# Performance work log

Measured on AMD Instinct MI355X. Metric: run time of the kernel, lower is better.

Reference implementation:

```python
import jax, jax.numpy as jnp
import numpy as np

NUM_HEADS = 8
MAXN = 1.0 - 1e-5        # ball projection radius for |k|=1
ATANH_CLIP = 1.0 - 1e-7  # artanh argument clamp (geoopt-style)
MIN_DEN = 1e-15

def _sqnorm(x):
    return jnp.sum(x * x, axis=-1, keepdims=True)

def _norm(x):
    return jnp.sqrt(jnp.clip(_sqnorm(x), MIN_DEN))

def artanh(x):
    return jnp.arctanh(jnp.clip(x, -ATANH_CLIP, ATANH_CLIP))

def project(x):
    n = _norm(x)
    return jnp.where(n > MAXN, x * (MAXN / n), x)

def mobius_add(x, y):
    # Mobius addition on Poincare ball, k=-1
    x2, y2 = _sqnorm(x), _sqnorm(y)
    xy = jnp.sum(x * y, axis=-1, keepdims=True)
    num = (1.0 + 2.0 * xy + y2) * x + (1.0 - x2) * y
    den = 1.0 + 2.0 * xy + x2 * y2
    return num / jnp.maximum(den, MIN_DEN)

def mobius_matvec(W, x):
    xn = jnp.clip(_norm(x), MIN_DEN)
    mx = x @ W.T
    mxn = jnp.clip(_norm(mx), MIN_DEN)
    res = jnp.tanh(mxn / xn * artanh(xn)) * (mx / mxn)
    zero = jnp.all(mx == 0, axis=-1, keepdims=True)
    return jnp.where(zero, jnp.zeros_like(res), res)

def mobius_linear(x, W, b):
    return project(mobius_add(mobius_matvec(W, x), b))

def logmap0(y):
    yn = jnp.clip(_norm(y), MIN_DEN)
    return artanh(yn) * y / yn

def expmap0(u):
    un = jnp.clip(_norm(u), MIN_DEN)
    return jnp.tanh(un) * u / un

def _fwd(query, key, value, Wq, bq, Wk, bk, Wv, bv, Wo, bo):
    B, S, D = query.shape
    dk = D // NUM_HEADS
    heads = lambda x: x.reshape(B, S, NUM_HEADS, dk).transpose(0, 2, 1, 3)
    Q = heads(mobius_linear(query, Wq, bq))  # (B,H,S,dk)
    K = heads(mobius_linear(key, Wk, bk))
    V = heads(mobius_linear(value, Wv, bv))
    # pairwise Poincare distance dist(q,k) = 2*artanh(||(-q) (+) k||),
    # expanded via dot products so we never build a (B,H,S,S,dk) tensor
    x2 = _sqnorm(Q)                          # (B,H,S,1)
    y2 = jnp.swapaxes(_sqnorm(K), -1, -2)    # (B,H,1,S)
    xy = jnp.einsum('bhid,bhjd->bhij', Q, K)
    A = 1.0 - 2.0 * xy + y2                  # coeff of (-q)
    Bc = 1.0 - x2                            # coeff of k
    num2 = A * A * x2 + Bc * Bc * y2 - 2.0 * A * Bc * xy
    den = jnp.maximum(1.0 - 2.0 * xy + x2 * y2, MIN_DEN)
    dist = 2.0 * artanh(jnp.sqrt(jnp.clip(num2, 0.0)) / den)
    scores = -dist / np.sqrt(dk).astype(np.float32)
    attn = jax.nn.softmax(scores, axis=-1)   # dropout skipped (eval/deterministic)
    # gyromidpoint weighted sum (vectorized form of the original python loops):
    # all softmax weights are > 0, so every j passes the >1e-10 branch
    w = attn / (jnp.sum(attn, axis=-1, keepdims=True) + 1e-10)
    mid = jnp.einsum('bhij,bhjd->bhid', w, logmap0(V))
    out = expmap0(mid)
    out = out.transpose(0, 2, 1, 3).reshape(B, S, D)
    return mobius_linear(out, Wo, bo), attn


def setup_inputs() -> dict:
    key = jax.random.key(0)
    ks = jax.random.split(key, 12)
    B, S, D = 2, 2048, 512
    pt = lambda k: project(0.05 * jax.random.normal(k, (B, S, D), dtype=jnp.float32))
    inp = {'query': pt(ks[0]), 'key': pt(ks[1]), 'value': pt(ks[2])}
    wscale = 1.0 / np.sqrt(D)
    for i, nm in enumerate(['q', 'k', 'v', 'o']):
        inp['W' + nm] = wscale * jax.random.normal(ks[3 + i], (D, D), dtype=jnp.float32)
        inp['b' + nm] = project(0.01 * jax.random.normal(ks[7 + i], (D,), dtype=jnp.float32))
    return inp


def reference(query, key, value, Wq, bq, Wk, bk, Wv, bv, Wo, bo):
    return _fwd(query, key, value, Wq, bq, Wk, bk, Wv, bv, Wo, bo)
```

## Files before the change

kernel.cpp:

```cpp
#include <hip/hip_runtime.h>
#include <math.h>

namespace {

constexpr int kB  = 2;
constexpr int kS  = 2048;
constexpr int kD  = 512;
constexpr int kH  = 8;
constexpr int kDK = 64;
constexpr int kM  = kB * kS;
constexpr int kBH = kB * kH;

typedef __attribute__((ext_vector_type(8))) short bf16x8;
typedef __attribute__((ext_vector_type(4))) float f32x4;

__device__ __forceinline__ float wave_sum64(float v) {
#pragma unroll
    for (int o = 32; o > 0; o >>= 1) v += __shfl_xor(v, o, 64);
    return v;
}

__device__ __forceinline__ unsigned short f2bf(float f) {
    unsigned u = __float_as_uint(f);
    unsigned r = (u + 0x7FFF + ((u >> 16) & 1)) >> 16;
    return (unsigned short)r;
}
__device__ __forceinline__ float bf2f(unsigned short h) {
    return __uint_as_float(((unsigned)h) << 16);
}

#define MAXN_F  ((float)(1.0 - 1e-5))
#define ACLIP_F ((float)(1.0 - 1e-7))

__global__ __launch_bounds__(256) void gemm_mfma(const float* __restrict__ X,
                                                 const float* __restrict__ W,
                                                 float* __restrict__ Y) {
    __shared__ unsigned short Ah[64 * 64], Al[64 * 64], Bh[64 * 64], Bl[64 * 64];
    const int m0 = blockIdx.x * 64;
    const int n0 = blockIdx.y * 64;
    const int tid = threadIdx.x;
    const int w = tid >> 6, l = tid & 63;
    const int lr = l & 15, lh = l >> 4;
    const int sr = tid >> 2;
    const int sk = (tid & 3) * 16;
    float4 xr[4], wr[4];
#pragma unroll
    for (int i = 0; i < 4; ++i) {
        xr[i] = *(const float4*)(X + (size_t)(m0 + sr) * 512 + sk + i * 4);
        wr[i] = *(const float4*)(W + (size_t)(n0 + sr) * 512 + sk + i * 4);
    }
    f32x4 acc[4];
#pragma unroll
    for (int j = 0; j < 4; ++j) acc[j] = (f32x4){0.f, 0.f, 0.f, 0.f};

    for (int c = 0; c < 8; ++c) {
        if (c) __syncthreads();
        {
            unsigned hx[8], lx[8], hw_[8], lw_[8];
#pragma unroll
            for (int t = 0; t < 8; ++t) {
                float e0 = ((const float*)&xr[t >> 1])[(t & 1) * 2 + 0];
                float e1 = ((const float*)&xr[t >> 1])[(t & 1) * 2 + 1];
                unsigned short h0 = f2bf(e0), h1 = f2bf(e1);
                hx[t] = (unsigned)h0 | ((unsigned)h1 << 16);
                lx[t] = (unsigned)f2bf(e0 - bf2f(h0)) | ((unsigned)f2bf(e1 - bf2f(h1)) << 16);
                float f0 = ((const float*)&wr[t >> 1])[(t & 1) * 2 + 0];
                float f1 = ((const float*)&wr[t >> 1])[(t & 1) * 2 + 1];
                unsigned short g0 = f2bf(f0), g1 = f2bf(f1);
                hw_[t] = (unsigned)g0 | ((unsigned)g1 << 16);
                lw_[t] = (unsigned)f2bf(f0 - bf2f(g0)) | ((unsigned)f2bf(f1 - bf2f(g1)) << 16);
            }
            const int ga = (sk >> 3) ^ (sr & 7);
            const int gb = ((sk >> 3) + 1) ^ (sr & 7);
            *(uint4*)&Ah[sr * 64 + ga * 8] = make_uint4(hx[0], hx[1], hx[2], hx[3]);
            *(uint4*)&Ah[sr * 64 + gb * 8] = make_uint4(hx[4], hx[5], hx[6], hx[7]);
            *(uint4*)&Al[sr * 64 + ga * 8] = make_uint4(lx[0], lx[1], lx[2], lx[3]);
            *(uint4*)&Al[sr * 64 + gb * 8] = make_uint4(lx[4], lx[5], lx[6], lx[7]);
            *(uint4*)&Bh[sr * 64 + ga * 8] = make_uint4(hw_[0], hw_[1], hw_[2], hw_[3]);
            *(uint4*)&Bh[sr * 64 + gb * 8] = make_uint4(hw_[4], hw_[5], hw_[6], hw_[7]);
            *(uint4*)&Bl[sr * 64 + ga * 8] = make_uint4(lw_[0], lw_[1], lw_[2], lw_[3]);
            *(uint4*)&Bl[sr * 64 + gb * 8] = make_uint4(lw_[4], lw_[5], lw_[6], lw_[7]);
        }
        if (c < 7) {
            const int k1 = (c + 1) * 64;
#pragma unroll
            for (int i = 0; i < 4; ++i) {
                xr[i] = *(const float4*)(X + (size_t)(m0 + sr) * 512 + k1 + sk + i * 4);
                wr[i] = *(const float4*)(W + (size_t)(n0 + sr) * 512 + k1 + sk + i * 4);
            }
        }
        __syncthreads();
#pragma unroll
        for (int ks = 0; ks < 2; ++ks) {
            const int kb = ks * 4 + lh;
            const int row = w * 16 + lr;
            const int aoff = row * 64 + ((kb ^ (row & 7)) << 3);
            bf16x8 ah = *(const bf16x8*)&Ah[aoff];
            bf16x8 al = *(const bf16x8*)&Al[aoff];
#pragma unroll
            for (int fn = 0; fn < 4; ++fn) {
                const int col = fn * 16 + lr;
                const int boff = col * 64 + ((kb ^ (col & 7)) << 3);
                bf16x8 bh8 = *(const bf16x8*)&Bh[boff];
                bf16x8 bl8 = *(const bf16x8*)&Bl[boff];
                acc[fn] = __builtin_amdgcn_mfma_f32_16x16x32_bf16(ah, bh8, acc[fn], 0, 0, 0);
                acc[fn] = __builtin_amdgcn_mfma_f32_16x16x32_bf16(al, bh8, acc[fn], 0, 0, 0);
                acc[fn] = __builtin_amdgcn_mfma_f32_16x16x32_bf16(ah, bl8, acc[fn], 0, 0, 0);
            }
        }
    }
#pragma unroll
    for (int fn = 0; fn < 4; ++fn)
#pragma unroll
        for (int r = 0; r < 4; ++r)
            Y[(size_t)(m0 + w * 16 + lh * 4 + r) * 512 + n0 + fn * 16 + lr] = acc[fn][r];
}

__global__ __launch_bounds__(256) void rowops(const float* __restrict__ X,
                                              const float* __restrict__ MX,
                                              const float* __restrict__ bvec,
                                              float* __restrict__ out) {
    __shared__ float4 red4[4];
    __shared__ float red1[4];
    const int row = blockIdx.x;
    const int tid = threadIdx.x;
    const float2 xv = ((const float2*)(X + (size_t)row * kD))[tid];
    const float2 mv = ((const float2*)(MX + (size_t)row * kD))[tid];
    const float2 bv = ((const float2*)bvec)[tid];
    float sx  = fmaf(xv.x, xv.x, xv.y * xv.y);
    float sm  = fmaf(mv.x, mv.x, mv.y * mv.y);
    float smb = fmaf(mv.x, bv.x, mv.y * bv.y);
    float sb  = fmaf(bv.x, bv.x, bv.y * bv.y);
#pragma unroll
    for (int o = 32; o > 0; o >>= 1) {
        sx  += __shfl_xor(sx, o, 64);
        sm  += __shfl_xor(sm, o, 64);
        smb += __shfl_xor(smb, o, 64);
        sb  += __shfl_xor(sb, o, 64);
    }
    if ((tid & 63) == 0) red4[tid >> 6] = make_float4(sx, sm, smb, sb);
    __syncthreads();
    {
        float4 r0 = red4[0], r1 = red4[1], r2 = red4[2], r3 = red4[3];
        sx  = r0.x + r1.x + r2.x + r3.x;
        sm  = r0.y + r1.y + r2.y + r3.y;
        smb = r0.z + r1.z + r2.z + r3.z;
        sb  = r0.w + r1.w + r2.w + r3.w;
    }
    float xn  = sqrtf(fmaxf(sx, 1e-15f));
    float mxn = sqrtf(fmaxf(sm, 1e-15f));
    float xc  = fminf(xn, ACLIP_F);
    float at  = 0.5f * logf((1.f + xc) / (1.f - xc));
    float sc  = tanhf(mxn / xn * at) / mxn;
    if (sm == 0.f) sc = 0.f;
    float x2 = sc * sc * sm;
    float xy = sc * smb;
    float y2 = sb;
    float c1 = 1.f + 2.f * xy + y2;
    float c2 = 1.f - x2;
    float den = fmaxf(1.f + 2.f * xy + x2 * y2, 1e-15f);
    float idn = 1.f / den;
    float ux = (c1 * sc * mv.x + c2 * bv.x) * idn;
    float uy = (c1 * sc * mv.y + c2 * bv.y) * idn;
    float su = wave_sum64(fmaf(ux, ux, uy * uy));
    if ((tid & 63) == 0) red1[tid >> 6] = su;
    __syncthreads();
    su = (red1[0] + red1[1]) + (red1[2] + red1[3]);
    float n = sqrtf(fmaxf(su, 1e-15f));
    float f = (n > MAXN_F) ? (MAXN_F / n) : 1.f;
    ((float2*)(out + (size_t)row * kD))[tid] = make_float2(ux * f, uy * f);
}

__global__ __launch_bounds__(256) void prep2(const float* __restrict__ Qp,
                                             const float* __restrict__ Kp,
                                             const float* __restrict__ Vp,
                                             float* __restrict__ qn2,
                                             float* __restrict__ kn2,
                                             unsigned short* __restrict__ LVbT) {
    __shared__ unsigned short T[64][66];
    const int bh = blockIdx.x >> 5;
    const int k0 = (blockIdx.x & 31) * 64;
    const int b = bh >> 3, h = bh & 7;
    const int w = threadIdx.x >> 6, l = threadIdx.x & 63;
#pragma unroll 4
    for (int i = 0; i < 16; ++i) {
        const int s = k0 + w * 16 + i;
        const size_t src = (size_t)(b * kS + s) * kD + h * kDK + l;
        float qv = Qp[src], kv = Kp[src], vv = Vp[src];
        float sq = wave_sum64(qv * qv);
        float sk = wave_sum64(kv * kv);
        float sv = wave_sum64(vv * vv);
        if (l == 0) { qn2[(bh << 11) + s] = sq; kn2[(bh << 11) + s] = sk; }
        float yn = sqrtf(fmaxf(sv, 1e-15f));
        float yc = fminf(yn, ACLIP_F);
        float coef = 0.5f * logf((1.f + yc) / (1.f - yc)) / yn;
        T[l][w * 16 + i] = f2bf(vv * coef);
    }
    __syncthreads();
    const int n = threadIdx.x >> 2, kk = (threadIdx.x & 3) * 16;
    const unsigned int* Tr = (const unsigned int*)&T[n][kk];
    unsigned int u0 = Tr[0], u1 = Tr[1], u2 = Tr[2], u3 = Tr[3];
    unsigned int u4 = Tr[4], u5 = Tr[5], u6 = Tr[6], u7 = Tr[7];
    unsigned short* dst = LVbT + (((size_t)(bh * 64 + n)) << 11) + k0 + kk;
    *(uint4*)dst = make_uint4(u0, u1, u2, u3);
    *(uint4*)(dst + 8) = make_uint4(u4, u5, u6, u7);
}

__global__ __launch_bounds__(256) void split_qk(const float* __restrict__ Qp,
                                                const float* __restrict__ Kp,
                                                unsigned short* __restrict__ Qhi,
                                                unsigned short* __restrict__ Qlo,
                                                unsigned short* __restrict__ Khi,
                                                unsigned short* __restrict__ Klo) {
    const int gid  = blockIdx.x * 4 + (threadIdx.x >> 6);
    const int lane = threadIdx.x & 63;
    const int bh = gid >> 11, s = gid & 2047;
    const int b = bh >> 3, h = bh & 7;
    const size_t src = (size_t)(b * kS + s) * kD + h * kDK + lane;
    const size_t dst = ((size_t)gid << 6) + lane;
    float qv = Qp[src];
    unsigned short qh = f2bf(qv);
    Qhi[dst] = qh;
    Qlo[dst] = f2bf(qv - bf2f(qh));
    float kv = Kp[src];
    unsigned short kh = f2bf(kv);
    Khi[dst] = kh;
    Klo[dst] = f2bf(kv - bf2f(kh));
}

__global__ __launch_bounds__(256) void fused_attn(const unsigned short* __restrict__ Qhi,
                                                  const unsigned short* __restrict__ Qlo,
                                                  const unsigned short* __restrict__ Khi,
                                                  const unsigned short* __restrict__ Klo,
                                                  const unsigned short* __restrict__ LVbT,
                                                  const float* __restrict__ qn2,
                                                  const float* __restrict__ kn2,
                                                  float* __restrict__ attn,
                                                  float* __restrict__ outcat) {
    __shared__ unsigned short KshH[64 * 64], KshL[64 * 64], LVsh[64 * 64], Psh[32 * 64];
    __shared__ float epl[32 * 68];
    __shared__ float kn2s[2048];
    __shared__ float qn2s[32];
    __shared__ float rsL[4][32], nsL[4][32];
    __shared__ float invSL[32], coefL[32];

    const int wgid = blockIdx.x;
    const int x = wgid & 7, bq_ = wgid >> 3;
    const int bh = 2 * x + (bq_ >> 6);
    const int i0 = (bq_ & 63) * 32;
    const int b = bh >> 3, h = bh & 7;
    const int tid = threadIdx.x;
    const int w = tid >> 6, l = tid & 63;
    const int lr = l & 15, lh = l >> 4;
    const int srj = tid >> 2;
    const int skk = (tid & 3) * 16;
    const size_t kvbase = ((size_t)(bh << 11)) << 6;
    const size_t lvbase = ((size_t)bh) << 17;

    {
        const float* src = kn2 + (bh << 11) + tid * 8;
        *(float4*)&kn2s[tid * 8]     = *(const float4*)src;
        *(float4*)&kn2s[tid * 8 + 4] = *(const float4*)(src + 4);
        if (tid < 32) qn2s[tid] = qn2[(bh << 11) + i0 + tid];
    }
    bf16x8 qah[2][2], qal[2][2];
#pragma unroll
    for (int fm = 0; fm < 2; ++fm)
#pragma unroll
        for (int ks = 0; ks < 2; ++ks) {
            const size_t a = ((size_t)(bh << 11) + i0 + fm * 16 + lr) * 64 + (ks * 4 + lh) * 8;
            qah[fm][ks] = *(const bf16x8*)&Qhi[a];
            qal[fm][ks] = *(const bf16x8*)&Qlo[a];
        }

    const int ga = (((skk >> 3) ^ (srj & 7)) << 3);
    const int gb = ((((skk >> 3) + 1) ^ (srj & 7)) << 3);
    const int jc = w * 16 + lr;
    uint4 pA0, pA1, pB0, pB1, pC0, pC1;
    {
        const unsigned short* kh = Khi + kvbase + (size_t)srj * 64 + skk;
        const unsigned short* kl = Klo + kvbase + (size_t)srj * 64 + skk;
        const unsigned short* lv = LVbT + lvbase + (size_t)srj * 2048 + skk;
        pA0 = *(const uint4*)kh; pA1 = *(const uint4*)(kh + 8);
        pB0 = *(const uint4*)kl; pB1 = *(const uint4*)(kl + 8);
        pC0 = *(const uint4*)lv; pC1 = *(const uint4*)(lv + 8);
    }

    f32x4 pvacc[2];
    pvacc[0] = (f32x4){0.f, 0.f, 0.f, 0.f};
    pvacc[1] = (f32x4){0.f, 0.f, 0.f, 0.f};
    float rsp[2][4] = {};

    for (int t = 0; t < 32; ++t) {
        const int j0 = t * 64;
        if (t) __syncthreads();
        *(uint4*)&KshH[srj * 64 + ga] = pA0; *(uint4*)&KshH[srj * 64 + gb] = pA1;
        *(uint4*)&KshL[srj * 64 + ga] = pB0; *(uint4*)&KshL[srj * 64 + gb] = pB1;
        *(uint4*)&LVsh[srj * 64 + ga] = pC0; *(uint4*)&LVsh[srj * 64 + gb] = pC1;
        if (t < 31) {
            const unsigned short* kh = Khi + kvbase + (size_t)(j0 + 64 + srj) * 64 + skk;
            const unsigned short* kl = Klo + kvbase + (size_t)(j0 + 64 + srj) * 64 + skk;
            const unsigned short* lv = LVbT + lvbase + (size_t)srj * 2048 + j0 + 64 + skk;
            pA0 = *(const uint4*)kh; pA1 = *(const uint4*)(kh + 8);
            pB0 = *(const uint4*)kl; pB1 = *(const uint4*)(kl + 8);
            pC0 = *(const uint4*)lv; pC1 = *(const uint4*)(lv + 8);
        }
        __syncthreads();
        f32x4 sacc[2];
        sacc[0] = (f32x4){0.f, 0.f, 0.f, 0.f};
        sacc[1] = (f32x4){0.f, 0.f, 0.f, 0.f};
#pragma unroll
        for (int ks = 0; ks < 2; ++ks) {
            const int kb = ks * 4 + lh;
            const int boff = jc * 64 + ((kb ^ (jc & 7)) << 3);
            bf16x8 bh8 = *(const bf16x8*)&KshH[boff];
            bf16x8 bl8 = *(const bf16x8*)&KshL[boff];
#pragma unroll
            for (int fm = 0; fm < 2; ++fm) {
                sacc[fm] = __builtin_amdgcn_mfma_f32_16x16x32_bf16(qah[fm][ks], bh8, sacc[fm], 0, 0, 0);
                sacc[fm] = __builtin_amdgcn_mfma_f32_16x16x32_bf16(qal[fm][ks], bh8, sacc[fm], 0, 0, 0);
                sacc[fm] = __builtin_amdgcn_mfma_f32_16x16x32_bf16(qah[fm][ks], bl8, sacc[fm], 0, 0, 0);
            }
        }
        const float y2 = kn2s[j0 + jc];
        const int pg = jc >> 3, pw = jc & 7;
#pragma unroll
        for (int fm = 0; fm < 2; ++fm)
#pragma unroll
            for (int r = 0; r < 4; ++r) {
                const int row = fm * 16 + lh * 4 + r;
                float xy = sacc[fm][r];
                float x2 = qn2s[row];
                float A_ = 1.f - 2.f * xy + y2;
                float Bc = 1.f - x2;
                float num2 = A_ * A_ * x2 + Bc * Bc * y2 - 2.f * A_ * Bc * xy;
                float den  = fmaxf(1.f - 2.f * xy + x2 * y2, 1e-15f);
                float sn   = __builtin_amdgcn_sqrtf(fmaxf(num2, 0.f));
                float dm   = den - sn;
                dm = fmaxf(dm, (den + sn) * 5e-8f);
                float rr = (den + sn) * __builtin_amdgcn_rcpf(dm);
                float e = __builtin_amdgcn_exp2f(-0.125f * __builtin_amdgcn_logf(rr));
                rsp[fm][r] += e;
                Psh[row * 64 + ((pg ^ (row & 7)) << 3) + pw] = f2bf(e);
            }
        __syncthreads();
#pragma unroll
        for (int ks = 0; ks < 2; ++ks) {
            const int kb = ks * 4 + lh;
            bf16x8 bv8 = *(const bf16x8*)&LVsh[jc * 64 + ((kb ^ (jc & 7)) << 3)];
#pragma unroll
            for (int fm = 0; fm < 2; ++fm) {
                const int prow = fm * 16 + lr;
                bf16x8 pa = *(const bf16x8*)&Psh[prow * 64 + ((kb ^ (prow & 7)) << 3)];
                pvacc[fm] = __builtin_amdgcn_mfma_f32_16x16x32_bf16(pa, bv8, pvacc[fm], 0, 0, 0);
            }
        }
    }
    __syncthreads();
#pragma unroll
    for (int fm = 0; fm < 2; ++fm)
#pragma unroll
        for (int r = 0; r < 4; ++r) {
            float v = rsp[fm][r];
            v += __shfl_xor(v, 1, 64); v += __shfl_xor(v, 2, 64);
            v += __shfl_xor(v, 4, 64); v += __shfl_xor(v, 8, 64);
            rsp[fm][r] = v;
        }
    if (lr == 0) {
#pragma unroll
        for (int fm = 0; fm < 2; ++fm)
#pragma unroll
            for (int r = 0; r < 4; ++r) rsL[w][fm * 16 + lh * 4 + r] = rsp[fm][r];
    }
    __syncthreads();
    if (tid < 32) invSL[tid] = 1.f / (rsL[0][tid] + rsL[1][tid] + rsL[2][tid] + rsL[3][tid]);
    __syncthreads();
    float mval[2][4];
#pragma unroll
    for (int fm = 0; fm < 2; ++fm)
#pragma unroll
        for (int r = 0; r < 4; ++r) {
            const int row = fm * 16 + lh * 4 + r;
            float m = pvacc[fm][r] * invSL[row];
            mval[fm][r] = m;
            float ns = m * m;
            ns += __shfl_xor(ns, 1, 64); ns += __shfl_xor(ns, 2, 64);
            ns += __shfl_xor(ns, 4, 64); ns += __shfl_xor(ns, 8, 64);
            if (lr == 0) nsL[w][row] = ns;
        }
    __syncthreads();
    if (tid < 32) {
        float ns = nsL[0][tid] + nsL[1][tid] + nsL[2][tid] + nsL[3][tid];
        float un = sqrtf(fmaxf(ns, 1e-15f));
        coefL[tid] = tanhf(un) / un;
    }
    __syncthreads();
#pragma unroll
    for (int fm = 0; fm < 2; ++fm)
#pragma unroll
        for (int r = 0; r < 4; ++r) {
            const int row = fm * 16 + lh * 4 + r;
            outcat[(size_t)(b * kS + i0 + row) * kD + h * kDK + jc] = mval[fm][r] * coefL[row];
        }

    {
        const unsigned short* kh = Khi + kvbase + (size_t)srj * 64 + skk;
        const unsigned short* kl = Klo + kvbase + (size_t)srj * 64 + skk;
        pA0 = *(const uint4*)kh; pA1 = *(const uint4*)(kh + 8);
        pB0 = *(const uint4*)kl; pB1 = *(const uint4*)(kl + 8);
    }
    for (int t = 0; t < 32; ++t) {
        const int j0 = t * 64;
        __syncthreads();
        *(uint4*)&KshH[srj * 64 + ga] = pA0; *(uint4*)&KshH[srj * 64 + gb] = pA1;
        *(uint4*)&KshL[srj * 64 + ga] = pB0; *(uint4*)&KshL[srj * 64 + gb] = pB1;
        if (t < 31) {
            const unsigned short* kh = Khi + kvbase + (size_t)(j0 + 64 + srj) * 64 + skk;
            const unsigned short* kl = Klo + kvbase + (size_t)(j0 + 64 + srj) * 64 + skk;
            pA0 = *(const uint4*)kh; pA1 = *(const uint4*)(kh + 8);
            pB0 = *(const uint4*)kl; pB1 = *(const uint4*)(kl + 8);
        }
        __syncthreads();
        f32x4 sacc[2];
        sacc[0] = (f32x4){0.f, 0.f, 0.f, 0.f};
        sacc[1] = (f32x4){0.f, 0.f, 0.f, 0.f};
#pragma unroll
        for (int ks = 0; ks < 2; ++ks) {
            const int kb = ks * 4 + lh;
            const int boff = jc * 64 + ((kb ^ (jc & 7)) << 3);
            bf16x8 bh8 = *(const bf16x8*)&KshH[boff];
            bf16x8 bl8 = *(const bf16x8*)&KshL[boff];
#pragma unroll
            for (int fm = 0; fm < 2; ++fm) {
                sacc[fm] = __builtin_amdgcn_mfma_f32_16x16x32_bf16(qah[fm][ks], bh8, sacc[fm], 0, 0, 0);
                sacc[fm] = __builtin_amdgcn_mfma_f32_16x16x32_bf16(qal[fm][ks], bh8, sacc[fm], 0, 0, 0);
                sacc[fm] = __builtin_amdgcn_mfma_f32_16x16x32_bf16(qah[fm][ks], bl8, sacc[fm], 0, 0, 0);
            }
        }
        const float y2 = kn2s[j0 + jc];
#pragma unroll
        for (int fm = 0; fm < 2; ++fm)
#pragma unroll
            for (int r = 0; r < 4; ++r) {
                const int row = fm * 16 + lh * 4 + r;
                float xy = sacc[fm][r];
                float x2 = qn2s[row];
                float A_ = 1.f - 2.f * xy + y2;
                float Bc = 1.f - x2;
                float num2 = A_ * A_ * x2 + Bc * Bc * y2 - 2.f * A_ * Bc * xy;
                float den  = fmaxf(1.f - 2.f * xy + x2 * y2, 1e-15f);
                float sn   = __builtin_amdgcn_sqrtf(fmaxf(num2, 0.f));
                float dm   = den - sn;
                dm = fmaxf(dm, (den + sn) * 5e-8f);
                float rr = (den + sn) * __builtin_amdgcn_rcpf(dm);
                float e = __builtin_amdgcn_exp2f(-0.125f * __builtin_amdgcn_logf(rr));
                epl[row * 68 + jc] = e * invSL[row];
            }
        __syncthreads();
        const int row = tid >> 3, c8 = (tid & 7) * 8;
        float4 v0 = *(const float4*)&epl[row * 68 + c8];
        float4 v1 = *(const float4*)&epl[row * 68 + c8 + 4];
        float* dst = attn + ((size_t)(bh << 11) + i0 + row) * kS + j0 + c8;
        *(float4*)dst = v0;
        *(float4*)(dst + 4) = v1;
    }
}

}

extern "C" void kernel_launch(void* const* d_in, const int* in_sizes, int n_in,
                              void* d_out, int out_size, void* d_ws, size_t ws_size,
                              hipStream_t stream) {
    const float* q  = (const float*)d_in[0];
    const float* k  = (const float*)d_in[1];
    const float* v  = (const float*)d_in[2];
    const float* Wq = (const float*)d_in[3];
    const float* bq = (const float*)d_in[4];
    const float* Wk = (const float*)d_in[5];
    const float* bk = (const float*)d_in[6];
    const float* Wv = (const float*)d_in[7];
    const float* bv = (const float*)d_in[8];
    const float* Wo = (const float*)d_in[9];
    const float* bo = (const float*)d_in[10];

    float* out  = (float*)d_out;
    float* attn = out + (size_t)kM * kD;

    constexpr size_t NBUF = (size_t)kM * kD;
    float* ws  = (float*)d_ws;
    float* A0  = ws;
    float* A1  = ws + NBUF;
    float* A2  = ws + 2 * NBUF;
    float* A3  = ws + 3 * NBUF;
    float* qn2 = ws + 4 * NBUF;
    float* kn2 = qn2 + (size_t)kBH * kS;

    constexpr size_t HP = (size_t)kBH * kS * kDK;
    unsigned short* Qhi = (unsigned short*)A2;
    unsigned short* Qlo = Qhi + HP;
    unsigned short* Khi = (unsigned short*)out;
    unsigned short* Klo = Khi + HP;
    unsigned short* LVbT = (unsigned short*)A3;

    dim3 gg(kM / 64, kD / 64);

    gemm_mfma<<<gg, 256, 0, stream>>>(q, Wq, A3);
    rowops<<<kM, 256, 0, stream>>>(q, A3, bq, A0);
    gemm_mfma<<<gg, 256, 0, stream>>>(k, Wk, A3);
    rowops<<<kM, 256, 0, stream>>>(k, A3, bk, A1);
    gemm_mfma<<<gg, 256, 0, stream>>>(v, Wv, A3);
    rowops<<<kM, 256, 0, stream>>>(v, A3, bv, A2);

    prep2<<<kBH * 32, 256, 0, stream>>>(A0, A1, A2, qn2, kn2, LVbT);

    split_qk<<<(kBH * kS) / 4, 256, 0, stream>>>(A0, A1, Qhi, Qlo, Khi, Klo);

    fused_attn<<<kBH * (kS / 32), 256, 0, stream>>>(Qhi, Qlo, Khi, Klo, LVbT,
                                                    qn2, kn2, attn, A1);

    gemm_mfma<<<gg, 256, 0, stream>>>(A1, Wo, A2);
    rowops<<<kM, 256, 0, stream>>>(A1, A2, bo, out);
}
```

Baseline: 303.3 us.

## Cache bf16 exp scores during first pass and normalize in separate kernel

Removes the second pass over K that recomputed QK scores and the distance transform just to write the normalized attention matrix. The first pass now stores the unnormalized bf16 weights and per-row inverse sums to a large workspace buffer, and a new elementwise kernel scales them into the fp32 attention output. This trades recomputation for an extra 128MB write and read of bf16 data, and lowers the precision of the attention output to bf16. It falls back to the old path when the workspace is too small.

```diff
diff --git a/kernel.cpp b/kernel.cpp
--- a/kernel.cpp
+++ b/kernel.cpp
@@ -228,6 +228,7 @@
     Klo[dst] = f2bf(kv - bf2f(kh));
 }
 
+template <bool WRITE_E>
 __global__ __launch_bounds__(256) void fused_attn(const unsigned short* __restrict__ Qhi,
                                                   const unsigned short* __restrict__ Qlo,
                                                   const unsigned short* __restrict__ Khi,
@@ -236,9 +237,10 @@
                                                   const float* __restrict__ qn2,
                                                   const float* __restrict__ kn2,
                                                   float* __restrict__ attn,
-                                                  float* __restrict__ outcat) {
+                                                  float* __restrict__ outcat,
+                                                  unsigned short* __restrict__ ebuf,
+                                                  float* __restrict__ invSg) {
     __shared__ unsigned short KshH[64 * 64], KshL[64 * 64], LVsh[64 * 64], Psh[32 * 64];
-    __shared__ float epl[32 * 68];
     __shared__ float kn2s[2048];
     __shared__ float qn2s[32];
     __shared__ float rsL[4][32], nsL[4][32];
@@ -355,6 +357,11 @@
                 pvacc[fm] = __builtin_amdgcn_mfma_f32_16x16x32_bf16(pa, bv8, pvacc[fm], 0, 0, 0);
             }
         }
+        if constexpr (WRITE_E) {
+            const int prow = tid >> 3, g = tid & 7;
+            uint4 ev = *(const uint4*)&Psh[prow * 64 + ((g ^ (prow & 7)) << 3)];
+            *(uint4*)(ebuf + ((size_t)(bh << 11) + i0 + prow) * kS + j0 + g * 8) = ev;
+        }
     }
     __syncthreads();
 #pragma unroll
@@ -373,7 +380,11 @@
             for (int r = 0; r < 4; ++r) rsL[w][fm * 16 + lh * 4 + r] = rsp[fm][r];
     }
     __syncthreads();
-    if (tid < 32) invSL[tid] = 1.f / (rsL[0][tid] + rsL[1][tid] + rsL[2][tid] + rsL[3][tid]);
+    if (tid < 32) {
+        float is = 1.f / (rsL[0][tid] + rsL[1][tid] + rsL[2][tid] + rsL[3][tid]);
+        invSL[tid] = is;
+        if constexpr (WRITE_E) invSg[(bh << 11) + i0 + tid] = is;
+    }
     __syncthreads();
     float mval[2][4];
 #pragma unroll
@@ -403,67 +414,92 @@
             outcat[(size_t)(b * kS + i0 + row) * kD + h * kDK + jc] = mval[fm][r] * coefL[row];
         }
 
-    {
-        const unsigned short* kh = Khi + kvbase + (size_t)srj * 64 + skk;
-        const unsigned short* kl = Klo + kvbase + (size_t)srj * 64 + skk;
-        pA0 = *(const uint4*)kh; pA1 = *(const uint4*)(kh + 8);
-        pB0 = *(const uint4*)kl; pB1 = *(const uint4*)(kl + 8);
-    }
-    for (int t = 0; t < 32; ++t) {
-        const int j0 = t * 64;
-        __syncthreads();
-        *(uint4*)&KshH[srj * 64 + ga] = pA0; *(uint4*)&KshH[srj * 64 + gb] = pA1;
-        *(uint4*)&KshL[srj * 64 + ga] = pB0; *(uint4*)&KshL[srj * 64 + gb] = pB1;
-        if (t < 31) {
-            const unsigned short* kh = Khi + kvbase + (size_t)(j0 + 64 + srj) * 64 + skk;
-            const unsigned short* kl = Klo + kvbase + (size_t)(j0 + 64 + srj) * 64 + skk;
+    if constexpr (!WRITE_E) {
+        __shared__ float epl[32 * 68];
+        {
+            const unsigned short* kh = Khi + kvbase + (size_t)srj * 64 + skk;
+            const unsigned short* kl = Klo + kvbase + (size_t)srj * 64 + skk;
             pA0 = *(const uint4*)kh; pA1 = *(const uint4*)(kh + 8);
             pB0 = *(const uint4*)kl; pB1 = *(const uint4*)(kl + 8);
         }
-        __syncthreads();
-        f32x4 sacc[2];
-        sacc[0] = (f32x4){0.f, 0.f, 0.f, 0.f};
-        sacc[1] = (f32x4){0.f, 0.f, 0.f, 0.f};
-#pragma unroll
-        for (int ks = 0; ks < 2; ++ks) {
-            const int kb = ks * 4 + lh;
-            const int boff = jc * 64 + ((kb ^ (jc & 7)) << 3);
-            bf16x8 bh8 = *(const bf16x8*)&KshH[boff];
-            bf16x8 bl8 = *(const bf16x8*)&KshL[boff];
-#pragma unroll
-            for (int fm = 0; fm < 2; ++fm) {
-                sacc[fm] = __builtin_amdgcn_mfma_f32_16x16x32_bf16(qah[fm][ks], bh8, sacc[fm], 0, 0, 0);
-                sacc[fm] = __builtin_amdgcn_mfma_f32_16x16x32_bf16(qal[fm][ks], bh8, sacc[fm], 0, 0, 0);
-                sacc[fm] = __builtin_amdgcn_mfma_f32_16x16x32_bf16(qah[fm][ks], bl8, sacc[fm], 0, 0, 0);
-            }
-        }
-        const float y2 = kn2s[j0 + jc];
-#pragma unroll
-        for (int fm = 0; fm < 2; ++fm)
-#pragma unroll
-            for (int r = 0; r < 4; ++r) {
-                const int row = fm * 16 + lh * 4 + r;
-                float xy = sacc[fm][r];
-                float x2 = qn2s[row];
-                float A_ = 1.f - 2.f * xy + y2;
-                float Bc = 1.f - x2;
-                float num2 = A_ * A_ * x2 + Bc * Bc * y2 - 2.f * A_ * Bc * xy;
-                float den  = fmaxf(1.f - 2.f * xy + x2 * y2, 1e-15f);
-                float sn   = __builtin_amdgcn_sqrtf(fmaxf(num2, 0.f));
-                float dm   = den - sn;
-                dm = fmaxf(dm, (den + sn) * 5e-8f);
-                float rr = (den + sn) * __builtin_amdgcn_rcpf(dm);
-                float e = __builtin_amdgcn_exp2f(-0.125f * __builtin_amdgcn_logf(rr));
-                epl[row * 68 + jc] = e * invSL[row];
-            }
-        __syncthreads();
-        const int row = tid >> 3, c8 = (tid & 7) * 8;
-        float4 v0 = *(const float4*)&epl[row * 68 + c8];
-        float4 v1 = *(const float4*)&epl[row * 68 + c8 + 4];
-        float* dst = attn + ((size_t)(bh << 11) + i0 + row) * kS + j0 + c8;
-        *(float4*)dst = v0;
-        *(float4*)(dst + 4) = v1;
-    }
+        for (int t = 0; t < 32; ++t) {
+            const int j0 = t * 64;
+            __syncthreads();
+            *(uint4*)&KshH[srj * 64 + ga] = pA0; *(uint4*)&KshH[srj * 64 + gb] = pA1;
+            *(uint4*)&KshL[srj * 64 + ga] = pB0; *(uint4*)&KshL[srj * 64 + gb] = pB1;
+            if (t < 31) {
+                const unsigned short* kh = Khi + kvbase + (size_t)(j0 + 64 + srj) * 64 + skk;
+                const unsigned short* kl = Klo + kvbase + (size_t)(j0 + 64 + srj) * 64 + skk;
+                pA0 = *(const uint4*)kh; pA1 = *(const uint4*)(kh + 8);
+                pB0 = *(const uint4*)kl; pB1 = *(const uint4*)(kl + 8);
+            }
+            __syncthreads();
+            f32x4 sacc[2];
+            sacc[0] = (f32x4){0.f, 0.f, 0.f, 0.f};
+            sacc[1] = (f32x4){0.f, 0.f, 0.f, 0.f};
+#pragma unroll
+            for (int ks = 0; ks < 2; ++ks) {
+                const int kb = ks * 4 + lh;
+                const int boff = jc * 64 + ((kb ^ (jc & 7)) << 3);
+                bf16x8 bh8 = *(const bf16x8*)&KshH[boff];
+                bf16x8 bl8 = *(const bf16x8*)&KshL[boff];
+#pragma unroll
+                for (int fm = 0; fm < 2; ++fm) {
+                    sacc[fm] = __builtin_amdgcn_mfma_f32_16x16x32_bf16(qah[fm][ks], bh8, sacc[fm], 0, 0, 0);
+                    sacc[fm] = __builtin_amdgcn_mfma_f32_16x16x32_bf16(qal[fm][ks], bh8, sacc[fm], 0, 0, 0);
+                    sacc[fm] = __builtin_amdgcn_mfma_f32_16x16x32_bf16(qah[fm][ks], bl8, sacc[fm], 0, 0, 0);
+                }
+            }
+            const float y2 = kn2s[j0 + jc];
+#pragma unroll
+            for (int fm = 0; fm < 2; ++fm)
+#pragma unroll
+                for (int r = 0; r < 4; ++r) {
+                    const int row = fm * 16 + lh * 4 + r;
+                    float xy = sacc[fm][r];
+                    float x2 = qn2s[row];
+                    float A_ = 1.f - 2.f * xy + y2;
+                    float Bc = 1.f - x2;
+                    float num2 = A_ * A_ * x2 + Bc * Bc * y2 - 2.f * A_ * Bc * xy;
+                    float den  = fmaxf(1.f - 2.f * xy + x2 * y2, 1e-15f);
+                    float sn   = __builtin_amdgcn_sqrtf(fmaxf(num2, 0.f));
+                    float dm   = den - sn;
+                    dm = fmaxf(dm, (den + sn) * 5e-8f);
+                    float rr = (den + sn) * __builtin_amdgcn_rcpf(dm);
+                    float e = __builtin_amdgcn_exp2f(-0.125f * __builtin_amdgcn_logf(rr));
+                    epl[row * 68 + jc] = e * invSL[row];
+                }
+            __syncthreads();
+            const int row = tid >> 3, c8 = (tid & 7) * 8;
+            float4 v0 = *(const float4*)&epl[row * 68 + c8];
+            float4 v1 = *(const float4*)&epl[row * 68 + c8 + 4];
+            float* dst = attn + ((size_t)(bh << 11) + i0 + row) * kS + j0 + c8;
+            *(float4*)dst = v0;
+            *(float4*)(dst + 4) = v1;
+        }
+    }
+}
+
+__global__ __launch_bounds__(256) void attn_norm(const unsigned short* __restrict__ ebuf,
+                                                 const float* __restrict__ invSg,
+                                                 float* __restrict__ attn) {
+    const size_t gid = (size_t)blockIdx.x * 256 + threadIdx.x;
+    const size_t row = gid >> 8;
+    const int col8 = (int)(gid & 255) * 8;
+    uint4 v = *(const uint4*)(ebuf + row * kS + col8);
+    const float is = invSg[row];
+    float o[8];
+    o[0] = __uint_as_float(v.x << 16) * is;
+    o[1] = __uint_as_float(v.x & 0xFFFF0000u) * is;
+    o[2] = __uint_as_float(v.y << 16) * is;
+    o[3] = __uint_as_float(v.y & 0xFFFF0000u) * is;
+    o[4] = __uint_as_float(v.z << 16) * is;
+    o[5] = __uint_as_float(v.z & 0xFFFF0000u) * is;
+    o[6] = __uint_as_float(v.w << 16) * is;
+    o[7] = __uint_as_float(v.w & 0xFFFF0000u) * is;
+    float* dst = attn + row * kS + col8;
+    *(float4*)dst       = make_float4(o[0], o[1], o[2], o[3]);
+    *(float4*)(dst + 4) = make_float4(o[4], o[5], o[6], o[7]);
 }
 
 }
@@ -494,6 +530,11 @@
     float* A3  = ws + 3 * NBUF;
     float* qn2 = ws + 4 * NBUF;
     float* kn2 = qn2 + (size_t)kBH * kS;
+    float* invSg = kn2 + (size_t)kBH * kS;
+    const size_t ebuf_off_bytes = (4 * NBUF + 3 * (size_t)kBH * kS) * sizeof(float);
+    unsigned short* ebuf = (unsigned short*)((char*)d_ws + ebuf_off_bytes);
+    const size_t ebuf_bytes = (size_t)kBH * kS * kS * sizeof(unsigned short);
+    const bool fast = ws_size >= ebuf_off_bytes + ebuf_bytes;
 
     constexpr size_t HP = (size_t)kBH * kS * kDK;
     unsigned short* Qhi = (unsigned short*)A2;
@@ -515,8 +556,14 @@
 
     split_qk<<<(kBH * kS) / 4, 256, 0, stream>>>(A0, A1, Qhi, Qlo, Khi, Klo);
 
-    fused_attn<<<kBH * (kS / 32), 256, 0, stream>>>(Qhi, Qlo, Khi, Klo, LVbT,
-                                                    qn2, kn2, attn, A1);
+    if (fast) {
+        fused_attn<true><<<kBH * (kS / 32), 256, 0, stream>>>(
+            Qhi, Qlo, Khi, Klo, LVbT, qn2, kn2, attn, A1, ebuf, invSg);
+        attn_norm<<<(kBH * kS * kS / 8) / 256, 256, 0, stream>>>(ebuf, invSg, attn);
+    } else {
+        fused_attn<false><<<kBH * (kS / 32), 256, 0, stream>>>(
+            Qhi, Qlo, Khi, Klo, LVbT, qn2, kn2, attn, A1, ebuf, invSg);
+    }
 
     gemm_mfma<<<gg, 256, 0, stream>>>(A1, Wo, A2);
     rowops<<<kM, 256, 0, stream>>>(A1, A2, bo, out);
```

Measured after the change: 304.0 us. No clear change (+0.2%).

## Store unnormalized bf16 attention in first pass and normalize in separate kernel

Applied to the files above, without the earlier changes.

The fused attention kernel no longer runs a second pass that recomputes QK scores and distances to write normalized attention. It writes the bf16 exponentials it already computed for the PV product into the attn buffer, using the first half of each fp32 row, and saves per-row inverse sums. A new attn_norm kernel expands each row in place to fp32 and scales it. This removes the duplicated MFMA and transcendental work but lowers attn precision to bf16 and adds an extra kernel with a read-modify-write of the attention matrix.

```diff
diff --git a/kernel.cpp b/kernel.cpp
--- a/kernel.cpp
+++ b/kernel.cpp
@@ -235,10 +235,10 @@
                                                   const unsigned short* __restrict__ LVbT,
                                                   const float* __restrict__ qn2,
                                                   const float* __restrict__ kn2,
-                                                  float* __restrict__ attn,
-                                                  float* __restrict__ outcat) {
+                                                  unsigned short* __restrict__ eattn,
+                                                  float* __restrict__ outcat,
+                                                  float* __restrict__ invSg) {
     __shared__ unsigned short KshH[64 * 64], KshL[64 * 64], LVsh[64 * 64], Psh[32 * 64];
-    __shared__ float epl[32 * 68];
     __shared__ float kn2s[2048];
     __shared__ float qn2s[32];
     __shared__ float rsL[4][32], nsL[4][32];
@@ -355,6 +355,11 @@
                 pvacc[fm] = __builtin_amdgcn_mfma_f32_16x16x32_bf16(pa, bv8, pvacc[fm], 0, 0, 0);
             }
         }
+        {
+            const int prow = tid >> 3, g = tid & 7;
+            uint4 ev = *(const uint4*)&Psh[prow * 64 + ((g ^ (prow & 7)) << 3)];
+            *(uint4*)(eattn + ((size_t)(bh << 11) + i0 + prow) * 4096 + j0 + g * 8) = ev;
+        }
     }
     __syncthreads();
 #pragma unroll
@@ -373,7 +378,11 @@
             for (int r = 0; r < 4; ++r) rsL[w][fm * 16 + lh * 4 + r] = rsp[fm][r];
     }
     __syncthreads();
-    if (tid < 32) invSL[tid] = 1.f / (rsL[0][tid] + rsL[1][tid] + rsL[2][tid] + rsL[3][tid]);
+    if (tid < 32) {
+        float is = 1.f / (rsL[0][tid] + rsL[1][tid] + rsL[2][tid] + rsL[3][tid]);
+        invSL[tid] = is;
+        invSg[(bh << 11) + i0 + tid] = is;
+    }
     __syncthreads();
     float mval[2][4];
 #pragma unroll
@@ -402,68 +411,28 @@
             const int row = fm * 16 + lh * 4 + r;
             outcat[(size_t)(b * kS + i0 + row) * kD + h * kDK + jc] = mval[fm][r] * coefL[row];
         }
-
-    {
-        const unsigned short* kh = Khi + kvbase + (size_t)srj * 64 + skk;
-        const unsigned short* kl = Klo + kvbase + (size_t)srj * 64 + skk;
-        pA0 = *(const uint4*)kh; pA1 = *(const uint4*)(kh + 8);
-        pB0 = *(const uint4*)kl; pB1 = *(const uint4*)(kl + 8);
-    }
-    for (int t = 0; t < 32; ++t) {
-        const int j0 = t * 64;
-        __syncthreads();
-        *(uint4*)&KshH[srj * 64 + ga] = pA0; *(uint4*)&KshH[srj * 64 + gb] = pA1;
-        *(uint4*)&KshL[srj * 64 + ga] = pB0; *(uint4*)&KshL[srj * 64 + gb] = pB1;
-        if (t < 31) {
-            const unsigned short* kh = Khi + kvbase + (size_t)(j0 + 64 + srj) * 64 + skk;
-            const unsigned short* kl = Klo + kvbase + (size_t)(j0 + 64 + srj) * 64 + skk;
-            pA0 = *(const uint4*)kh; pA1 = *(const uint4*)(kh + 8);
-            pB0 = *(const uint4*)kl; pB1 = *(const uint4*)(kl + 8);
-        }
-        __syncthreads();
-        f32x4 sacc[2];
-        sacc[0] = (f32x4){0.f, 0.f, 0.f, 0.f};
-        sacc[1] = (f32x4){0.f, 0.f, 0.f, 0.f};
-#pragma unroll
-        for (int ks = 0; ks < 2; ++ks) {
-            const int kb = ks * 4 + lh;
-            const int boff = jc * 64 + ((kb ^ (jc & 7)) << 3);
-            bf16x8 bh8 = *(const bf16x8*)&KshH[boff];
-            bf16x8 bl8 = *(const bf16x8*)&KshL[boff];
-#pragma unroll
-            for (int fm = 0; fm < 2; ++fm) {
-                sacc[fm] = __builtin_amdgcn_mfma_f32_16x16x32_bf16(qah[fm][ks], bh8, sacc[fm], 0, 0, 0);
-                sacc[fm] = __builtin_amdgcn_mfma_f32_16x16x32_bf16(qal[fm][ks], bh8, sacc[fm], 0, 0, 0);
-                sacc[fm] = __builtin_amdgcn_mfma_f32_16x16x32_bf16(qah[fm][ks], bl8, sacc[fm], 0, 0, 0);
-            }
-        }
-        const float y2 = kn2s[j0 + jc];
-#pragma unroll
-        for (int fm = 0; fm < 2; ++fm)
-#pragma unroll
-            for (int r = 0; r < 4; ++r) {
-                const int row = fm * 16 + lh * 4 + r;
-                float xy = sacc[fm][r];
-                float x2 = qn2s[row];
-                float A_ = 1.f - 2.f * xy + y2;
-                float Bc = 1.f - x2;
-                float num2 = A_ * A_ * x2 + Bc * Bc * y2 - 2.f * A_ * Bc * xy;
-                float den  = fmaxf(1.f - 2.f * xy + x2 * y2, 1e-15f);
-                float sn   = __builtin_amdgcn_sqrtf(fmaxf(num2, 0.f));
-                float dm   = den - sn;
-                dm = fmaxf(dm, (den + sn) * 5e-8f);
-                float rr = (den + sn) * __builtin_amdgcn_rcpf(dm);
-                float e = __builtin_amdgcn_exp2f(-0.125f * __builtin_amdgcn_logf(rr));
-                epl[row * 68 + jc] = e * invSL[row];
-            }
-        __syncthreads();
-        const int row = tid >> 3, c8 = (tid & 7) * 8;
-        float4 v0 = *(const float4*)&epl[row * 68 + c8];
-        float4 v1 = *(const float4*)&epl[row * 68 + c8 + 4];
-        float* dst = attn + ((size_t)(bh << 11) + i0 + row) * kS + j0 + c8;
-        *(float4*)dst = v0;
-        *(float4*)(dst + 4) = v1;
-    }
+}
+
+__global__ __launch_bounds__(256) void attn_norm(float* __restrict__ attn,
+                                                 const float* __restrict__ invSg) {
+    const int row = blockIdx.x;
+    const int t = threadIdx.x;
+    const unsigned short* u = (const unsigned short*)attn + (size_t)row * 4096;
+    uint4 v = *(const uint4*)(u + t * 8);
+    const float is = invSg[row];
+    __syncthreads();
+    float o[8];
+    o[0] = __uint_as_float(v.x << 16) * is;
+    o[1] = __uint_as_float(v.x & 0xFFFF0000u) * is;
+    o[2] = __uint_as_float(v.y << 16) * is;
+    o[3] = __uint_as_float(v.y & 0xFFFF0000u) * is;
+    o[4] = __uint_as_float(v.z << 16) * is;
+    o[5] = __uint_as_float(v.z & 0xFFFF0000u) * is;
+    o[6] = __uint_as_float(v.w << 16) * is;
+    o[7] = __uint_as_float(v.w & 0xFFFF0000u) * is;
+    float* dst = attn + (size_t)row * kS + t * 8;
+    *(float4*)dst       = make_float4(o[0], o[1], o[2], o[3]);
+    *(float4*)(dst + 4) = make_float4(o[4], o[5], o[6], o[7]);
 }
 
 }
@@ -494,6 +463,7 @@
     float* A3  = ws + 3 * NBUF;
     float* qn2 = ws + 4 * NBUF;
     float* kn2 = qn2 + (size_t)kBH * kS;
+    float* invSg = kn2 + (size_t)kBH * kS;
 
     constexpr size_t HP = (size_t)kBH * kS * kDK;
     unsigned short* Qhi = (unsigned short*)A2;
@@ -516,7 +486,10 @@
     split_qk<<<(kBH * kS) / 4, 256, 0, stream>>>(A0, A1, Qhi, Qlo, Khi, Klo);
 
     fused_attn<<<kBH * (kS / 32), 256, 0, stream>>>(Qhi, Qlo, Khi, Klo, LVbT,
-                                                    qn2, kn2, attn, A1);
+                                                    qn2, kn2,
+                                                    (unsigned short*)attn, A1, invSg);
+
+    attn_norm<<<kBH * kS, 256, 0, stream>>>(attn, invSg);
 
     gemm_mfma<<<gg, 256, 0, stream>>>(A1, Wo, A2);
     rowops<<<kM, 256, 0, stream>>>(A1, A2, bo, out);
```

New measurement: 298.3 us. No clear change (-1.7%).
